# Optimization experiments

Hardware: AMD Instinct MI355X
Metric: run time of the kernel (lower is better)

## Reference

```python
import jax, jax.numpy as jnp
import numpy as np

N = 50000
E = 800000
IN_DIM = 128
HID = 64
HEADS = 4
OUT_DIM = 128


def setup_inputs() -> dict:
    key = jax.random.key(0)
    ks = jax.random.split(key, 12)
    s = lambda fan: 1.0 / np.sqrt(fan)
    return {
        'features': jax.random.normal(ks[0], (N, IN_DIM), jnp.float32),
        'edge_index': jax.random.randint(ks[1], (2, E), 0, N, jnp.int64),
        # layer 1: in_dim -> heads*hid, concat=True
        'W1': jax.random.normal(ks[2], (IN_DIM, HEADS * HID), jnp.float32) * s(IN_DIM),
        'att_src1': jax.random.normal(ks[3], (HEADS, HID), jnp.float32) * s(HID),
        'att_dst1': jax.random.normal(ks[4], (HEADS, HID), jnp.float32) * s(HID),
        'bias1': jnp.zeros((HEADS * HID,), jnp.float32),
        # layer 2: heads*hid -> out_dim, 1 head, concat=False
        'W2': jax.random.normal(ks[5], (HEADS * HID, OUT_DIM), jnp.float32) * s(HEADS * HID),
        'att_src2': jax.random.normal(ks[6], (1, OUT_DIM), jnp.float32) * s(OUT_DIM),
        'att_dst2': jax.random.normal(ks[7], (1, OUT_DIM), jnp.float32) * s(OUT_DIM),
        'bias2': jnp.zeros((OUT_DIM,), jnp.float32),
    }


def _gat_conv(x, src, dst, W, a_src, a_dst, bias, heads, out_ch):
    n = x.shape[0]
    h = (x @ W).reshape(n, heads, out_ch)              # [N, H, C]
    alpha_s = jnp.einsum('nhc,hc->nh', h, a_src)       # [N, H]
    alpha_d = jnp.einsum('nhc,hc->nh', h, a_dst)
    e = jax.nn.leaky_relu(alpha_s[src] + alpha_d[dst], 0.2)  # [E, H]
    # segment softmax over incoming edges of each dst node
    m = jax.ops.segment_max(e, dst, num_segments=n)
    m = jnp.where(jnp.isfinite(m), m, 0.0)
    ex = jnp.exp(e - m[dst])
    denom = jax.ops.segment_sum(ex, dst, num_segments=n)
    alpha = ex / denom[dst]                            # [E, H]
    out = jax.ops.segment_sum(alpha[:, :, None] * h[src], dst, num_segments=n)  # [N, H, C]
    return out.reshape(n, heads * out_ch) + bias


def reference(features, edge_index, W1, att_src1, att_dst1, bias1, W2, att_src2, att_dst2, bias2):
    n = features.shape[0]
    loops = jnp.arange(n, dtype=edge_index.dtype)
    src = jnp.concatenate([edge_index[0], loops])
    dst = jnp.concatenate([edge_index[1], loops])

    act = lambda v: jax.nn.leaky_relu(v, 0.2)
    x = _gat_conv(features, src, dst, W1, att_src1, att_dst1, bias1, HEADS, HID)
    x = act(x)  # dropout inactive (eval)
    x = _gat_conv(x, src, dst, W2, att_src2, att_dst2, bias2, 1, OUT_DIM)
    x = act(x)
    # in_dim == out_dim -> identity residual
    return x + features
```

## Files before the change

kernel.cpp:

```cpp
#include <hip/hip_runtime.h>
#include <math.h>

#define LRELU(x) ((x) > 0.0f ? (x) : 0.2f * (x))

typedef __attribute__((ext_vector_type(8))) short bf16x8;
typedef __attribute__((ext_vector_type(4))) float floatx4;
typedef __attribute__((ext_vector_type(2))) float f32x2;

__device__ __forceinline__ float bf2f(ushort u) {
    union { unsigned u; float f; } v; v.u = ((unsigned)u) << 16; return v.f;
}
__device__ __forceinline__ ushort f2bf(float f) {
    union { float f; unsigned u; } v; v.f = f;
    unsigned r = (v.u + 0x7FFFu + ((v.u >> 16) & 1u)) >> 16;
    return (ushort)r;
}
__device__ __forceinline__ f32x2 bfpair(unsigned w) {
    union { unsigned u; float f; } lo, hi;
    lo.u = w << 16; hi.u = w & 0xffff0000u;
    return (f32x2){lo.f, hi.f};
}

__global__ __launch_bounds__(256) void prep_kernel(
    const float* __restrict__ feat, const float* __restrict__ W1,
    const float* __restrict__ as1, const float* __restrict__ ad1,
    const float* __restrict__ W2, const float* __restrict__ as2,
    const float* __restrict__ ad2, const int* __restrict__ ei,
    ushort* __restrict__ featb, ushort* __restrict__ Bp1, ushort* __restrict__ Bp2,
    int* __restrict__ deg, ushort* __restrict__ col,
    int N, int E, int Npart, int b_fil, int b_cvt, int b_p1)
{
    const int b = blockIdx.x, t = threadIdx.x;
    if (b < b_fil) {
        const int fb = b;
        const int part = fb & 7;
        const int base = (fb >> 3) * 2048;
        const int lo = part * Npart;
        const int hi = min(N, lo + Npart);
        for (int q0 = 0; q0 < 8; q0 += 4) {
            int dsts[4]; bool val[4];
#pragma unroll
            for (int u = 0; u < 4; ++u) {
                int k = base + (q0 + u) * 256 + t;
                val[u] = k < E;
                if (val[u]) dsts[u] = ei[E + k];
            }
#pragma unroll
            for (int u = 0; u < 4; ++u) {
                if (val[u] && dsts[u] >= lo && dsts[u] < hi) {
                    int k = base + (q0 + u) * 256 + t;
                    int src = ei[k];
                    int slot = atomicAdd(&deg[dsts[u]], 1);
                    if (slot < 63) col[dsts[u] * 64 + slot] = (ushort)src;
                }
            }
        }
    } else if (b < b_fil + b_cvt) {
        int i = (b - b_fil) * 256 + t;
        if (i < N * 32) {
            float4 v = ((const float4*)feat)[i];
            ushort4 o;
            o.x = f2bf(v.x); o.y = f2bf(v.y); o.z = f2bf(v.z); o.w = f2bf(v.w);
            ((ushort4*)featb)[i] = o;
        }
    } else if (b < b_fil + b_cvt + b_p1) {
        int i = (b - b_fil - b_cvt) * 256 + t;
        if (i < 272 * 128) {
            int n = i / 128, k = i % 128;
            float v;
            if (n < 256) v = W1[k * 256 + n];
            else if (n < 260) {
                int h = n - 256; float s = 0.f;
                for (int c = 0; c < 64; ++c) s += W1[k * 256 + h * 64 + c] * as1[h * 64 + c];
                v = s;
            } else if (n < 264) {
                int h = n - 260; float s = 0.f;
                for (int c = 0; c < 64; ++c) s += W1[k * 256 + h * 64 + c] * ad1[h * 64 + c];
                v = s;
            } else v = 0.f;
            Bp1[i] = f2bf(v);
        }
    } else {
        int i = (b - b_fil - b_cvt - b_p1) * 256 + t;
        if (i < 144 * 256) {
            int n = i / 256, k = i % 256;
            float v;
            if (n < 128) v = W2[k * 128 + n];
            else if (n == 128) {
                float s = 0.f;
                for (int c = 0; c < 128; ++c) s += W2[k * 128 + c] * as2[c];
                v = s;
            } else if (n == 129) {
                float s = 0.f;
                for (int c = 0; c < 128; ++c) s += W2[k * 128 + c] * ad2[c];
                v = s;
            } else v = 0.f;
            Bp2[i] = f2bf(v);
        }
    }
}

__global__ __launch_bounds__(256) void gemm_attn1_kernel(
    const ushort* __restrict__ A, const ushort* __restrict__ Bp,
    float* __restrict__ as_, float* __restrict__ ad_, int M)
{
    const int lane = threadIdx.x & 63;
    const int wave = threadIdx.x >> 6;
    const int quad = lane >> 4;
    const int l16  = lane & 15;
    const int row0 = blockIdx.x * 64 + wave * 16;
    const int arow = min(row0 + l16, M - 1);
    const ushort* ap = A + (size_t)arow * 128 + quad * 8;
    const ushort* bp = Bp + (size_t)(256 + l16) * 128 + quad * 8;

    floatx4 acc = (floatx4){0.f, 0.f, 0.f, 0.f};
#pragma unroll
    for (int k0 = 0; k0 < 128; k0 += 32) {
        bf16x8 a = *(const bf16x8*)(ap + k0);
        bf16x8 b = *(const bf16x8*)(bp + k0);
        acc = __builtin_amdgcn_mfma_f32_16x16x32_bf16(a, b, acc, 0, 0, 0);
    }
#pragma unroll
    for (int r = 0; r < 4; ++r) {
        int row = row0 + quad * 4 + r;
        if (row < M) {
            float v = acc[r];
            if (l16 < 4)      as_[row * 4 + l16] = v;
            else if (l16 < 8) ad_[row * 4 + (l16 - 4)] = v;
        }
    }
}

__global__ __launch_bounds__(256) void gat_gather1_kernel(
    const int* __restrict__ deg, const ushort* __restrict__ col,
    const float* __restrict__ as_, const float* __restrict__ ad_,
    const ushort* __restrict__ xb, ushort* __restrict__ aggx, int N)
{
    __shared__ float4 alph[4][64];
    const int lane = threadIdx.x & 63;
    const int wave = threadIdx.x >> 6;
    const int n = blockIdx.x * 4 + wave;
    if (n >= N) return;
    const int dgE = min(deg[n], 63);
    const float4 ad4 = *(const float4*)(ad_ + n * 4);

    int src = n;
    float4 ex4 = {0.f, 0.f, 0.f, 0.f};
    if (lane <= dgE) {
        if (lane < dgE) src = col[n * 64 + lane];
        float4 a4 = *(const float4*)(as_ + src * 4);
        ex4.x = __expf(LRELU(a4.x + ad4.x));
        ex4.y = __expf(LRELU(a4.y + ad4.y));
        ex4.z = __expf(LRELU(a4.z + ad4.z));
        ex4.w = __expf(LRELU(a4.w + ad4.w));
        alph[wave][lane] = ex4;
    }
    float sx = ex4.x, sy = ex4.y, sz = ex4.z, sw = ex4.w;
#pragma unroll
    for (int m = 1; m < 64; m <<= 1) {
        sx += __shfl_xor(sx, m, 64); sy += __shfl_xor(sy, m, 64);
        sz += __shfl_xor(sz, m, 64); sw += __shfl_xor(sw, m, 64);
    }
    const float rd0 = 1.0f / sx, rd1 = 1.0f / sy, rd2 = 1.0f / sz, rd3 = 1.0f / sw;

    const int esl = lane >> 5;
    const int ch0 = (lane & 31) * 4;
    const int dg = dgE + 1;
    f32x2 accA[4] = {{0.f,0.f},{0.f,0.f},{0.f,0.f},{0.f,0.f}};
    f32x2 accB[4] = {{0.f,0.f},{0.f,0.f},{0.f,0.f},{0.f,0.f}};

    for (int j0 = 0; j0 < dg; j0 += 8) {
        uint2 u[4]; float4 a[4]; bool v[4]; int jj[4];
#pragma unroll
        for (int q = 0; q < 4; ++q) {
            jj[q] = j0 + 2 * q + esl;
            v[q] = jj[q] < dg;
            if (v[q]) {
                int s = __shfl(src, jj[q], 64);
                a[q] = alph[wave][jj[q]];
                u[q] = *(const uint2*)(xb + (size_t)s * 128 + ch0);
            }
        }
#pragma unroll
        for (int q = 0; q < 4; ++q) {
            if (v[q]) {
                f32x2 xlo = bfpair(u[q].x), xhi = bfpair(u[q].y);
                accA[0] += (f32x2){a[q].x, a[q].x} * xlo; accB[0] += (f32x2){a[q].x, a[q].x} * xhi;
                accA[1] += (f32x2){a[q].y, a[q].y} * xlo; accB[1] += (f32x2){a[q].y, a[q].y} * xhi;
                accA[2] += (f32x2){a[q].z, a[q].z} * xlo; accB[2] += (f32x2){a[q].z, a[q].z} * xhi;
                accA[3] += (f32x2){a[q].w, a[q].w} * xlo; accB[3] += (f32x2){a[q].w, a[q].w} * xhi;
            }
        }
    }
#pragma unroll
    for (int h = 0; h < 4; ++h) {
        accA[h].x += __shfl_xor(accA[h].x, 32, 64); accA[h].y += __shfl_xor(accA[h].y, 32, 64);
        accB[h].x += __shfl_xor(accB[h].x, 32, 64); accB[h].y += __shfl_xor(accB[h].y, 32, 64);
    }

    if (lane < 32) {
        const float rd[4] = {rd0, rd1, rd2, rd3};
#pragma unroll
        for (int h = 0; h < 4; ++h) {
            ushort4 o;
            o.x = f2bf(accA[h].x * rd[h]); o.y = f2bf(accA[h].y * rd[h]);
            o.z = f2bf(accB[h].x * rd[h]); o.w = f2bf(accB[h].y * rd[h]);
            *(ushort4*)(aggx + ((size_t)h * N + n) * 128 + ch0) = o;
        }
    }
}

__device__ __forceinline__ void l2_tile(int ct, const ushort x1s[64][264],
    const ushort* __restrict__ Bp2, int brow, int M, int lane,
    ushort* __restrict__ h2b, float* __restrict__ as2_, float* __restrict__ ad2_)
{
    const int quad = lane >> 4;
    const int l16  = lane & 15;
    bf16x8 bfr[8];
#pragma unroll
    for (int kq = 0; kq < 8; ++kq)
        bfr[kq] = *(const bf16x8*)(Bp2 + (size_t)(ct * 16 + l16) * 256 + kq * 32 + quad * 8);

    floatx4 acc[4];
#pragma unroll
    for (int rg = 0; rg < 4; ++rg) acc[rg] = (floatx4){0.f, 0.f, 0.f, 0.f};
#pragma unroll
    for (int kq = 0; kq < 8; ++kq) {
#pragma unroll
        for (int rg = 0; rg < 4; ++rg) {
            bf16x8 a = *(const bf16x8*)&x1s[rg * 16 + l16][kq * 32 + quad * 8];
            acc[rg] = __builtin_amdgcn_mfma_f32_16x16x32_bf16(a, bfr[kq], acc[rg], 0, 0, 0);
        }
    }
    if (ct < 8) {
#pragma unroll
        for (int rg = 0; rg < 4; ++rg)
#pragma unroll
            for (int r = 0; r < 4; ++r) {
                int row = brow + rg * 16 + quad * 4 + r;
                if (row < M) h2b[(size_t)row * 128 + ct * 16 + l16] = f2bf(acc[rg][r]);
            }
    } else {
#pragma unroll
        for (int rg = 0; rg < 4; ++rg)
#pragma unroll
            for (int r = 0; r < 4; ++r) {
                int row = brow + rg * 16 + quad * 4 + r;
                if (row < M) {
                    if (l16 == 0)      as2_[row] = acc[rg][r];
                    else if (l16 == 1) ad2_[row] = acc[rg][r];
                }
            }
    }
}

__global__ __launch_bounds__(256) void gemm_l1l2_kernel(
    const ushort* __restrict__ aggx, const ushort* __restrict__ Bp1,
    const float* __restrict__ bias1, const ushort* __restrict__ Bp2,
    ushort* __restrict__ h2b, float* __restrict__ as2_, float* __restrict__ ad2_, int M)
{
    __shared__ ushort x1s[64][264];
    const int lane = threadIdx.x & 63;
    const int wave = threadIdx.x >> 6;
    const int quad = lane >> 4;
    const int l16  = lane & 15;
    const int brow = blockIdx.x * 64;

    bf16x8 bfr[4][4];
#pragma unroll
    for (int nt = 0; nt < 4; ++nt)
#pragma unroll
        for (int kq = 0; kq < 4; ++kq)
            bfr[nt][kq] = *(const bf16x8*)(Bp1 + (size_t)(wave * 64 + nt * 16 + l16) * 128 + kq * 32 + quad * 8);

    bf16x8 afr[4][4];
#pragma unroll
    for (int rt = 0; rt < 4; ++rt) {
        const int arow = min(brow + rt * 16 + l16, M - 1);
        const ushort* ap = aggx + ((size_t)wave * M + arow) * 128 + quad * 8;
#pragma unroll
        for (int kq = 0; kq < 4; ++kq)
            afr[rt][kq] = *(const bf16x8*)(ap + kq * 32);
    }

#pragma unroll
    for (int rt = 0; rt < 4; ++rt) {
        floatx4 acc[4];
#pragma unroll
        for (int nt = 0; nt < 4; ++nt) acc[nt] = (floatx4){0.f, 0.f, 0.f, 0.f};
#pragma unroll
        for (int kq = 0; kq < 4; ++kq)
#pragma unroll
            for (int nt = 0; nt < 4; ++nt)
                acc[nt] = __builtin_amdgcn_mfma_f32_16x16x32_bf16(afr[rt][kq], bfr[nt][kq], acc[nt], 0, 0, 0);
#pragma unroll
        for (int nt = 0; nt < 4; ++nt) {
            const int c = wave * 64 + nt * 16 + l16;
            const float bv = bias1[c];
#pragma unroll
            for (int r = 0; r < 4; ++r)
                x1s[rt * 16 + quad * 4 + r][c] = f2bf(LRELU(acc[nt][r] + bv));
        }
    }
    __syncthreads();

    l2_tile(wave * 2,     x1s, Bp2, brow, M, lane, h2b, as2_, ad2_);
    l2_tile(wave * 2 + 1, x1s, Bp2, brow, M, lane, h2b, as2_, ad2_);
    if (wave == 3)
        l2_tile(8,        x1s, Bp2, brow, M, lane, h2b, as2_, ad2_);
}

__global__ __launch_bounds__(256) void gat_gather2_kernel(
    const int* __restrict__ deg, const ushort* __restrict__ col,
    const float* __restrict__ as_, const float* __restrict__ ad_,
    const ushort* __restrict__ h2, const float* __restrict__ bias,
    const float* __restrict__ resid, float* __restrict__ out, int N)
{
    __shared__ float alph[4][64];
    const int lane = threadIdx.x & 63;
    const int wave = threadIdx.x >> 6;
    const int n = blockIdx.x * 4 + wave;
    if (n >= N) return;
    const int dgE = min(deg[n], 63);
    const float adv = ad_[n];

    int src = n;
    float ex = 0.f;
    if (lane <= dgE) {
        if (lane < dgE) src = col[n * 64 + lane];
        ex = __expf(LRELU(as_[src] + adv));
        alph[wave][lane] = ex;
    }
    float s = ex;
#pragma unroll
    for (int m = 1; m < 64; m <<= 1) s += __shfl_xor(s, m, 64);
    const float rden = 1.0f / s;

    const int esl = lane >> 5;
    const int ch0 = (lane & 31) * 4;
    const int dg = dgE + 1;
    f32x2 accA = {0.f, 0.f}, accB = {0.f, 0.f};

    for (int j0 = 0; j0 < dg; j0 += 8) {
        uint2 u[4]; float a[4]; bool v[4]; int jj[4];
#pragma unroll
        for (int q = 0; q < 4; ++q) {
            jj[q] = j0 + 2 * q + esl;
            v[q] = jj[q] < dg;
            if (v[q]) {
                int sA = __shfl(src, jj[q], 64);
                a[q] = alph[wave][jj[q]];
                u[q] = *(const uint2*)(h2 + (size_t)sA * 128 + ch0);
            }
        }
#pragma unroll
        for (int q = 0; q < 4; ++q) {
            if (v[q]) {
                accA += (f32x2){a[q], a[q]} * bfpair(u[q].x);
                accB += (f32x2){a[q], a[q]} * bfpair(u[q].y);
            }
        }
    }
    accA.x += __shfl_xor(accA.x, 32, 64); accA.y += __shfl_xor(accA.y, 32, 64);
    accB.x += __shfl_xor(accB.x, 32, 64); accB.y += __shfl_xor(accB.y, 32, 64);

    if (lane < 32) {
        const float4 bv = *(const float4*)(bias + ch0);
        const float4 fv = *(const float4*)(resid + (size_t)n * 128 + ch0);
        float4 o;
        o.x = LRELU(accA.x * rden + bv.x) + fv.x;
        o.y = LRELU(accA.y * rden + bv.y) + fv.y;
        o.z = LRELU(accB.x * rden + bv.z) + fv.z;
        o.w = LRELU(accB.y * rden + bv.w) + fv.w;
        *(float4*)(out + (size_t)n * 128 + ch0) = o;
    }
}

extern "C" void kernel_launch(void* const* d_in, const int* in_sizes, int n_in,
                              void* d_out, int out_size, void* d_ws, size_t ws_size,
                              hipStream_t stream)
{
    const float* feat = (const float*)d_in[0];
    const int*   ei   = (const int*)d_in[1];
    const float* W1   = (const float*)d_in[2];
    const float* asrc1 = (const float*)d_in[3];
    const float* adst1 = (const float*)d_in[4];
    const float* bias1 = (const float*)d_in[5];
    const float* W2    = (const float*)d_in[6];
    const float* asrc2 = (const float*)d_in[7];
    const float* adst2 = (const float*)d_in[8];
    const float* bias2 = (const float*)d_in[9];
    float* outp = (float*)d_out;

    const int IN_DIM = 128, C2 = 128;
    const int N = in_sizes[0] / IN_DIM;
    const int E = in_sizes[1] / 2;

    char* w = (char*)d_ws;
    ushort* featb = (ushort*)w; w += (size_t)N * IN_DIM * 2;
    ushort* aggx  = (ushort*)w; w += (size_t)4 * N * IN_DIM * 2;
    ushort* h2b   = (ushort*)w; w += (size_t)N * C2 * 2;
    ushort* Bp1   = (ushort*)w; w += (size_t)272 * 128 * 2;
    ushort* Bp2   = (ushort*)w; w += (size_t)144 * 256 * 2;
    float* as1_   = (float*)w;  w += (size_t)N * 4 * 4;
    float* ad1_   = (float*)w;  w += (size_t)N * 4 * 4;
    float* as2_   = (float*)w;  w += (size_t)N * 4;
    float* ad2_   = (float*)w;  w += (size_t)N * 4;
    int* deg      = (int*)w;    w += (size_t)N * 4;
    ushort* col   = (ushort*)w; w += (size_t)N * 64 * 2;

    dim3 blk(256);
    const int mg = (N + 63) / 64;
    const int gg = (N + 3) / 4;
    const int Npart = (N + 7) / 8;

    const int b_cvt = (N * 32 + 255) / 256;
    const int b_p1  = (272 * 128 + 255) / 256;
    const int b_p2  = (144 * 256 + 255) / 256;
    const int b_fil = 8 * ((E + 2047) / 2048);

    hipMemsetAsync(deg, 0, (size_t)N * 4, stream);
    prep_kernel<<<dim3(b_fil + b_cvt + b_p1 + b_p2), blk, 0, stream>>>(
        feat, W1, asrc1, adst1, W2, asrc2, adst2, ei,
        featb, Bp1, Bp2, deg, col, N, E, Npart, b_fil, b_cvt, b_p1);

    gemm_attn1_kernel<<<dim3(mg), blk, 0, stream>>>(featb, Bp1, as1_, ad1_, N);
    gat_gather1_kernel<<<dim3(gg), blk, 0, stream>>>(deg, col, as1_, ad1_, featb, aggx, N);

    gemm_l1l2_kernel<<<dim3(mg), blk, 0, stream>>>(aggx, Bp1, bias1, Bp2, h2b, as2_, ad2_, N);

    gat_gather2_kernel<<<dim3(gg), blk, 0, stream>>>(deg, col, as2_, ad2_, h2b, bias2, feat, outp, N);
}
```

Measured before the change: 255.5 us.

## Fuse layer-1 gather with layer-1 and layer-2 GEMMs into one kernel

Merges the layer-1 attention gather with the following GEMM kernel. Each block gathers 16 destination nodes into shared memory per head, then runs the W1 projection with bias and leaky-relu, then the W2 projection plus the attention logits. The goal is to stop writing and re-reading the 4×N×128 bf16 aggregated intermediate through global memory and to save a kernel launch. In exchange the GEMM tiles shrink from 64 to 16 rows, so the Bp1 and Bp2 weight fragments are reloaded far more often per row. The gather phase also runs four nodes per wave serially, which may lower memory-level parallelism.

```diff
diff --git a/kernel.cpp b/kernel.cpp
--- a/kernel.cpp
+++ b/kernel.cpp
@@ -7,9 +7,6 @@
 typedef __attribute__((ext_vector_type(4))) float floatx4;
 typedef __attribute__((ext_vector_type(2))) float f32x2;
 
-__device__ __forceinline__ float bf2f(ushort u) {
-    union { unsigned u; float f; } v; v.u = ((unsigned)u) << 16; return v.f;
-}
 __device__ __forceinline__ ushort f2bf(float f) {
     union { float f; unsigned u; } v; v.f = f;
     unsigned r = (v.u + 0x7FFFu + ((v.u >> 16) & 1u)) >> 16;
@@ -131,183 +128,160 @@
     }
 }
 
-__global__ __launch_bounds__(256) void gat_gather1_kernel(
+__global__ __launch_bounds__(256) void gat_fused1_kernel(
     const int* __restrict__ deg, const ushort* __restrict__ col,
     const float* __restrict__ as_, const float* __restrict__ ad_,
-    const ushort* __restrict__ xb, ushort* __restrict__ aggx, int N)
+    const ushort* __restrict__ xb, const ushort* __restrict__ Bp1,
+    const float* __restrict__ bias1, const ushort* __restrict__ Bp2,
+    ushort* __restrict__ h2b, float* __restrict__ as2_, float* __restrict__ ad2_, int N)
 {
     __shared__ float4 alph[4][64];
-    const int lane = threadIdx.x & 63;
-    const int wave = threadIdx.x >> 6;
-    const int n = blockIdx.x * 4 + wave;
-    if (n >= N) return;
-    const int dgE = min(deg[n], 63);
-    const float4 ad4 = *(const float4*)(ad_ + n * 4);
-
-    int src = n;
-    float4 ex4 = {0.f, 0.f, 0.f, 0.f};
-    if (lane <= dgE) {
-        if (lane < dgE) src = col[n * 64 + lane];
-        float4 a4 = *(const float4*)(as_ + src * 4);
-        ex4.x = __expf(LRELU(a4.x + ad4.x));
-        ex4.y = __expf(LRELU(a4.y + ad4.y));
-        ex4.z = __expf(LRELU(a4.z + ad4.z));
-        ex4.w = __expf(LRELU(a4.w + ad4.w));
-        alph[wave][lane] = ex4;
-    }
-    float sx = ex4.x, sy = ex4.y, sz = ex4.z, sw = ex4.w;
-#pragma unroll
-    for (int m = 1; m < 64; m <<= 1) {
-        sx += __shfl_xor(sx, m, 64); sy += __shfl_xor(sy, m, 64);
-        sz += __shfl_xor(sz, m, 64); sw += __shfl_xor(sw, m, 64);
-    }
-    const float rd0 = 1.0f / sx, rd1 = 1.0f / sy, rd2 = 1.0f / sz, rd3 = 1.0f / sw;
-
-    const int esl = lane >> 5;
-    const int ch0 = (lane & 31) * 4;
-    const int dg = dgE + 1;
-    f32x2 accA[4] = {{0.f,0.f},{0.f,0.f},{0.f,0.f},{0.f,0.f}};
-    f32x2 accB[4] = {{0.f,0.f},{0.f,0.f},{0.f,0.f},{0.f,0.f}};
-
-    for (int j0 = 0; j0 < dg; j0 += 8) {
-        uint2 u[4]; float4 a[4]; bool v[4]; int jj[4];
-#pragma unroll
-        for (int q = 0; q < 4; ++q) {
-            jj[q] = j0 + 2 * q + esl;
-            v[q] = jj[q] < dg;
-            if (v[q]) {
-                int s = __shfl(src, jj[q], 64);
-                a[q] = alph[wave][jj[q]];
-                u[q] = *(const uint2*)(xb + (size_t)s * 128 + ch0);
-            }
-        }
-#pragma unroll
-        for (int q = 0; q < 4; ++q) {
-            if (v[q]) {
-                f32x2 xlo = bfpair(u[q].x), xhi = bfpair(u[q].y);
-                accA[0] += (f32x2){a[q].x, a[q].x} * xlo; accB[0] += (f32x2){a[q].x, a[q].x} * xhi;
-                accA[1] += (f32x2){a[q].y, a[q].y} * xlo; accB[1] += (f32x2){a[q].y, a[q].y} * xhi;
-                accA[2] += (f32x2){a[q].z, a[q].z} * xlo; accB[2] += (f32x2){a[q].z, a[q].z} * xhi;
-                accA[3] += (f32x2){a[q].w, a[q].w} * xlo; accB[3] += (f32x2){a[q].w, a[q].w} * xhi;
-            }
-        }
-    }
-#pragma unroll
-    for (int h = 0; h < 4; ++h) {
-        accA[h].x += __shfl_xor(accA[h].x, 32, 64); accA[h].y += __shfl_xor(accA[h].y, 32, 64);
-        accB[h].x += __shfl_xor(accB[h].x, 32, 64); accB[h].y += __shfl_xor(accB[h].y, 32, 64);
-    }
-
-    if (lane < 32) {
-        const float rd[4] = {rd0, rd1, rd2, rd3};
-#pragma unroll
-        for (int h = 0; h < 4; ++h) {
-            ushort4 o;
-            o.x = f2bf(accA[h].x * rd[h]); o.y = f2bf(accA[h].y * rd[h]);
-            o.z = f2bf(accB[h].x * rd[h]); o.w = f2bf(accB[h].y * rd[h]);
-            *(ushort4*)(aggx + ((size_t)h * N + n) * 128 + ch0) = o;
-        }
-    }
-}
-
-__device__ __forceinline__ void l2_tile(int ct, const ushort x1s[64][264],
-    const ushort* __restrict__ Bp2, int brow, int M, int lane,
-    ushort* __restrict__ h2b, float* __restrict__ as2_, float* __restrict__ ad2_)
-{
-    const int quad = lane >> 4;
-    const int l16  = lane & 15;
-    bf16x8 bfr[8];
-#pragma unroll
-    for (int kq = 0; kq < 8; ++kq)
-        bfr[kq] = *(const bf16x8*)(Bp2 + (size_t)(ct * 16 + l16) * 256 + kq * 32 + quad * 8);
-
-    floatx4 acc[4];
-#pragma unroll
-    for (int rg = 0; rg < 4; ++rg) acc[rg] = (floatx4){0.f, 0.f, 0.f, 0.f};
-#pragma unroll
-    for (int kq = 0; kq < 8; ++kq) {
-#pragma unroll
-        for (int rg = 0; rg < 4; ++rg) {
-            bf16x8 a = *(const bf16x8*)&x1s[rg * 16 + l16][kq * 32 + quad * 8];
-            acc[rg] = __builtin_amdgcn_mfma_f32_16x16x32_bf16(a, bfr[kq], acc[rg], 0, 0, 0);
-        }
-    }
-    if (ct < 8) {
-#pragma unroll
-        for (int rg = 0; rg < 4; ++rg)
-#pragma unroll
-            for (int r = 0; r < 4; ++r) {
-                int row = brow + rg * 16 + quad * 4 + r;
-                if (row < M) h2b[(size_t)row * 128 + ct * 16 + l16] = f2bf(acc[rg][r]);
-            }
-    } else {
-#pragma unroll
-        for (int rg = 0; rg < 4; ++rg)
-#pragma unroll
-            for (int r = 0; r < 4; ++r) {
-                int row = brow + rg * 16 + quad * 4 + r;
-                if (row < M) {
-                    if (l16 == 0)      as2_[row] = acc[rg][r];
-                    else if (l16 == 1) ad2_[row] = acc[rg][r];
-                }
-            }
-    }
-}
-
-__global__ __launch_bounds__(256) void gemm_l1l2_kernel(
-    const ushort* __restrict__ aggx, const ushort* __restrict__ Bp1,
-    const float* __restrict__ bias1, const ushort* __restrict__ Bp2,
-    ushort* __restrict__ h2b, float* __restrict__ as2_, float* __restrict__ ad2_, int M)
-{
-    __shared__ ushort x1s[64][264];
+    __shared__ __align__(16) ushort agg[4][16][136];
+    __shared__ __align__(16) ushort x1s[16][264];
     const int lane = threadIdx.x & 63;
     const int wave = threadIdx.x >> 6;
     const int quad = lane >> 4;
     const int l16  = lane & 15;
-    const int brow = blockIdx.x * 64;
-
-    bf16x8 bfr[4][4];
-#pragma unroll
-    for (int nt = 0; nt < 4; ++nt)
-#pragma unroll
-        for (int kq = 0; kq < 4; ++kq)
-            bfr[nt][kq] = *(const bf16x8*)(Bp1 + (size_t)(wave * 64 + nt * 16 + l16) * 128 + kq * 32 + quad * 8);
-
-    bf16x8 afr[4][4];
-#pragma unroll
-    for (int rt = 0; rt < 4; ++rt) {
-        const int arow = min(brow + rt * 16 + l16, M - 1);
-        const ushort* ap = aggx + ((size_t)wave * M + arow) * 128 + quad * 8;
-#pragma unroll
-        for (int kq = 0; kq < 4; ++kq)
-            afr[rt][kq] = *(const bf16x8*)(ap + kq * 32);
-    }
-
-#pragma unroll
-    for (int rt = 0; rt < 4; ++rt) {
+    const int brow = blockIdx.x * 16;
+    const int esl = lane >> 5;
+    const int ch0 = (lane & 31) * 4;
+
+    for (int i = 0; i < 4; ++i) {
+        const int row = wave * 4 + i;
+        const int n = brow + row;
+        if (n < N) {
+            const int dgE = min(deg[n], 63);
+            const float4 ad4 = *(const float4*)(ad_ + n * 4);
+            int src = n;
+            float4 ex4 = {0.f, 0.f, 0.f, 0.f};
+            if (lane <= dgE) {
+                if (lane < dgE) src = col[n * 64 + lane];
+                float4 a4 = *(const float4*)(as_ + src * 4);
+                ex4.x = __expf(LRELU(a4.x + ad4.x));
+                ex4.y = __expf(LRELU(a4.y + ad4.y));
+                ex4.z = __expf(LRELU(a4.z + ad4.z));
+                ex4.w = __expf(LRELU(a4.w + ad4.w));
+                alph[wave][lane] = ex4;
+            }
+            float sx = ex4.x, sy = ex4.y, sz = ex4.z, sw = ex4.w;
+#pragma unroll
+            for (int m = 1; m < 64; m <<= 1) {
+                sx += __shfl_xor(sx, m, 64); sy += __shfl_xor(sy, m, 64);
+                sz += __shfl_xor(sz, m, 64); sw += __shfl_xor(sw, m, 64);
+            }
+            const float rd[4] = {1.0f / sx, 1.0f / sy, 1.0f / sz, 1.0f / sw};
+
+            const int dg = dgE + 1;
+            f32x2 accA[4] = {{0.f,0.f},{0.f,0.f},{0.f,0.f},{0.f,0.f}};
+            f32x2 accB[4] = {{0.f,0.f},{0.f,0.f},{0.f,0.f},{0.f,0.f}};
+            for (int j0 = 0; j0 < dg; j0 += 8) {
+                uint2 u[4]; float4 a[4]; bool v[4]; int jj[4];
+#pragma unroll
+                for (int q = 0; q < 4; ++q) {
+                    jj[q] = j0 + 2 * q + esl;
+                    v[q] = jj[q] < dg;
+                    if (v[q]) {
+                        int s = __shfl(src, jj[q], 64);
+                        a[q] = alph[wave][jj[q]];
+                        u[q] = *(const uint2*)(xb + (size_t)s * 128 + ch0);
+                    }
+                }
+#pragma unroll
+                for (int q = 0; q < 4; ++q) {
+                    if (v[q]) {
+                        f32x2 xlo = bfpair(u[q].x), xhi = bfpair(u[q].y);
+                        accA[0] += (f32x2){a[q].x, a[q].x} * xlo; accB[0] += (f32x2){a[q].x, a[q].x} * xhi;
+                        accA[1] += (f32x2){a[q].y, a[q].y} * xlo; accB[1] += (f32x2){a[q].y, a[q].y} * xhi;
+                        accA[2] += (f32x2){a[q].z, a[q].z} * xlo; accB[2] += (f32x2){a[q].z, a[q].z} * xhi;
+                        accA[3] += (f32x2){a[q].w, a[q].w} * xlo; accB[3] += (f32x2){a[q].w, a[q].w} * xhi;
+                    }
+                }
+            }
+#pragma unroll
+            for (int h = 0; h < 4; ++h) {
+                accA[h].x += __shfl_xor(accA[h].x, 32, 64); accA[h].y += __shfl_xor(accA[h].y, 32, 64);
+                accB[h].x += __shfl_xor(accB[h].x, 32, 64); accB[h].y += __shfl_xor(accB[h].y, 32, 64);
+            }
+            if (lane < 32) {
+#pragma unroll
+                for (int h = 0; h < 4; ++h) {
+                    ushort4 o;
+                    o.x = f2bf(accA[h].x * rd[h]); o.y = f2bf(accA[h].y * rd[h]);
+                    o.z = f2bf(accB[h].x * rd[h]); o.w = f2bf(accB[h].y * rd[h]);
+                    *(ushort4*)&agg[h][row][ch0] = o;
+                }
+            }
+        } else if (lane < 32) {
+            ushort4 z = {0, 0, 0, 0};
+#pragma unroll
+            for (int h = 0; h < 4; ++h) *(ushort4*)&agg[h][row][ch0] = z;
+        }
+    }
+    __syncthreads();
+
+    {
         floatx4 acc[4];
 #pragma unroll
         for (int nt = 0; nt < 4; ++nt) acc[nt] = (floatx4){0.f, 0.f, 0.f, 0.f};
 #pragma unroll
-        for (int kq = 0; kq < 4; ++kq)
-#pragma unroll
-            for (int nt = 0; nt < 4; ++nt)
-                acc[nt] = __builtin_amdgcn_mfma_f32_16x16x32_bf16(afr[rt][kq], bfr[nt][kq], acc[nt], 0, 0, 0);
+        for (int kq = 0; kq < 4; ++kq) {
+            bf16x8 a = *(const bf16x8*)&agg[wave][l16][kq * 32 + quad * 8];
+#pragma unroll
+            for (int nt = 0; nt < 4; ++nt) {
+                bf16x8 b = *(const bf16x8*)(Bp1 + (size_t)(wave * 64 + nt * 16 + l16) * 128 + kq * 32 + quad * 8);
+                acc[nt] = __builtin_amdgcn_mfma_f32_16x16x32_bf16(a, b, acc[nt], 0, 0, 0);
+            }
+        }
 #pragma unroll
         for (int nt = 0; nt < 4; ++nt) {
             const int c = wave * 64 + nt * 16 + l16;
             const float bv = bias1[c];
 #pragma unroll
             for (int r = 0; r < 4; ++r)
-                x1s[rt * 16 + quad * 4 + r][c] = f2bf(LRELU(acc[nt][r] + bv));
+                x1s[quad * 4 + r][c] = f2bf(LRELU(acc[nt][r] + bv));
         }
     }
     __syncthreads();
 
-    l2_tile(wave * 2,     x1s, Bp2, brow, M, lane, h2b, as2_, ad2_);
-    l2_tile(wave * 2 + 1, x1s, Bp2, brow, M, lane, h2b, as2_, ad2_);
-    if (wave == 3)
-        l2_tile(8,        x1s, Bp2, brow, M, lane, h2b, as2_, ad2_);
+#pragma unroll
+    for (int tt = 0; tt < 2; ++tt) {
+        const int ct = wave * 2 + tt;
+        bf16x8 bfr[8];
+#pragma unroll
+        for (int kq = 0; kq < 8; ++kq)
+            bfr[kq] = *(const bf16x8*)(Bp2 + (size_t)(ct * 16 + l16) * 256 + kq * 32 + quad * 8);
+        floatx4 acc = (floatx4){0.f, 0.f, 0.f, 0.f};
+#pragma unroll
+        for (int kq = 0; kq < 8; ++kq) {
+            bf16x8 a = *(const bf16x8*)&x1s[l16][kq * 32 + quad * 8];
+            acc = __builtin_amdgcn_mfma_f32_16x16x32_bf16(a, bfr[kq], acc, 0, 0, 0);
+        }
+#pragma unroll
+        for (int r = 0; r < 4; ++r) {
+            int row = brow + quad * 4 + r;
+            if (row < N) h2b[(size_t)row * 128 + ct * 16 + l16] = f2bf(acc[r]);
+        }
+    }
+    if (wave == 3) {
+        bf16x8 bfr[8];
+#pragma unroll
+        for (int kq = 0; kq < 8; ++kq)
+            bfr[kq] = *(const bf16x8*)(Bp2 + (size_t)(128 + l16) * 256 + kq * 32 + quad * 8);
+        floatx4 acc = (floatx4){0.f, 0.f, 0.f, 0.f};
+#pragma unroll
+        for (int kq = 0; kq < 8; ++kq) {
+            bf16x8 a = *(const bf16x8*)&x1s[l16][kq * 32 + quad * 8];
+            acc = __builtin_amdgcn_mfma_f32_16x16x32_bf16(a, bfr[kq], acc, 0, 0, 0);
+        }
+#pragma unroll
+        for (int r = 0; r < 4; ++r) {
+            int row = brow + quad * 4 + r;
+            if (row < N) {
+                if (l16 == 0)      as2_[row] = acc[r];
+                else if (l16 == 1) ad2_[row] = acc[r];
+            }
+        }
+    }
 }
 
 __global__ __launch_bounds__(256) void gat_gather2_kernel(
@@ -398,7 +372,6 @@
 
     char* w = (char*)d_ws;
     ushort* featb = (ushort*)w; w += (size_t)N * IN_DIM * 2;
-    ushort* aggx  = (ushort*)w; w += (size_t)4 * N * IN_DIM * 2;
     ushort* h2b   = (ushort*)w; w += (size_t)N * C2 * 2;
     ushort* Bp1   = (ushort*)w; w += (size_t)272 * 128 * 2;
     ushort* Bp2   = (ushort*)w; w += (size_t)144 * 256 * 2;
@@ -411,6 +384,7 @@
 
     dim3 blk(256);
     const int mg = (N + 63) / 64;
+    const int fg = (N + 15) / 16;
     const int gg = (N + 3) / 4;
     const int Npart = (N + 7) / 8;
 
@@ -425,9 +399,9 @@
         featb, Bp1, Bp2, deg, col, N, E, Npart, b_fil, b_cvt, b_p1);
 
     gemm_attn1_kernel<<<dim3(mg), blk, 0, stream>>>(featb, Bp1, as1_, ad1_, N);
-    gat_gather1_kernel<<<dim3(gg), blk, 0, stream>>>(deg, col, as1_, ad1_, featb, aggx, N);
-
-    gemm_l1l2_kernel<<<dim3(mg), blk, 0, stream>>>(aggx, Bp1, bias1, Bp2, h2b, as2_, ad2_, N);
+
+    gat_fused1_kernel<<<dim3(fg), blk, 0, stream>>>(
+        deg, col, as1_, ad1_, featb, Bp1, bias1, Bp2, h2b, as2_, ad2_, N);
 
     gat_gather2_kernel<<<dim3(gg), blk, 0, stream>>>(deg, col, as2_, ad2_, h2b, bias2, feat, outp, N);
 }
```

Result: slower. 286.5 us (+12.2%).
